# Kernel optimization log

Measured on AMD Instinct MI355X. Metric: run time of the kernel, lower is better.

Reference implementation:

```python
import jax, jax.numpy as jnp
import numpy as np

BN_EPS = 1e-5


def setup_inputs() -> dict:
    key = jax.random.key(0)
    ks = jax.random.split(key, 10)
    B, C, Ci, H, W = 4, 256, 128, 64, 64
    s = 0.05
    return {
        "x": jax.random.normal(ks[0], (B, C, H, W), jnp.float32),
        "g_w": jax.random.normal(ks[1], (Ci, C), jnp.float32) * s,
        "g_b": jax.random.normal(ks[2], (Ci,), jnp.float32) * s,
        "theta_w": jax.random.normal(ks[3], (Ci, C), jnp.float32) * s,
        "theta_b": jax.random.normal(ks[4], (Ci,), jnp.float32) * s,
        "phi_w": jax.random.normal(ks[5], (Ci, C), jnp.float32) * s,
        "phi_b": jax.random.normal(ks[6], (Ci,), jnp.float32) * s,
        "W_w": jax.random.normal(ks[7], (C, Ci), jnp.float32) * s,
        "W_b": jax.random.normal(ks[8], (C,), jnp.float32) * s,
        "bn_gamma": jnp.ones((C,), jnp.float32),
        "bn_beta": jnp.zeros((C,), jnp.float32),
        "scale": jax.random.normal(ks[9], (1,), jnp.float32),
    }


def reference(x, g_w, g_b, theta_w, theta_b, phi_w, phi_b, W_w, W_b, bn_gamma, bn_beta, scale):
    B, C, H, W = x.shape
    xf = x.reshape(B, C, H * W)  # [B, C, N]
    # 1x1 conv projections == channel matmuls
    g = jnp.einsum('oc,bcn->bno', g_w, xf) + g_b            # [B, N, Ci]
    th = jnp.einsum('oc,bcn->bno', theta_w, xf) + theta_b   # [B, N, Ci]
    ph = jnp.einsum('oc,bcn->bon', phi_w, xf) + phi_b[:, None]  # [B, Ci, N]
    # unscaled attention: f = theta @ phi, softmax over keys
    f = jnp.einsum('bnd,bdm->bnm', th, ph)                  # [B, N, N]
    attn = jax.nn.softmax(f, axis=-1)
    y = jnp.einsum('bnm,bmo->bno', attn, g)                 # [B, N, Ci]
    y4 = y.transpose(0, 2, 1).reshape(B, -1, H, W)          # [B, Ci, H, W]
    # W: 1x1 conv + BatchNorm2d (training mode: batch statistics)
    wy = jnp.einsum('od,bdhw->bohw', W_w, y4) + W_b[None, :, None, None]
    mean = wy.mean(axis=(0, 2, 3))
    var = wy.var(axis=(0, 2, 3))
    bn = (wy - mean[None, :, None, None]) * jax.lax.rsqrt(var[None, :, None, None] + BN_EPS)
    bn = bn * bn_gamma[None, :, None, None] + bn_beta[None, :, None, None]
    return scale * bn + x
```

## Files before the change

kernel.cpp:

```cpp
#include <hip/hip_runtime.h>
#include <hip/hip_bf16.h>

#define BB 4
#define CC 256
#define CI 128
#define NN 4096

typedef _Float16 f16;
typedef __attribute__((ext_vector_type(8))) _Float16 f16x8;
typedef __attribute__((ext_vector_type(4))) _Float16 f16x4;
typedef __attribute__((ext_vector_type(4))) float f32x4;

#define MFMA(a,b,c) __builtin_amdgcn_mfma_f32_16x16x32_f16(a,b,c,0,0,0)
#define LDS3(p) ((__attribute__((address_space(3))) void*)(p))
#define GL1(p)  ((const __attribute__((address_space(1))) void*)(p))

__global__ __launch_bounds__(256) void k01_xpose(const float* x, f16* xt,
                                                 const float* tw, const float* pw,
                                                 const float* gw, const float* Ww, f16* wdst){
    int nt = blockIdx.x, ct = blockIdx.y, b = blockIdx.z;
    __shared__ float tile[64][65];
    int t = threadIdx.x;
    const float* src = x + ((size_t)(b*CC + ct*64))*NN + nt*64;
    #pragma unroll
    for (int k=0;k<16;k++){ int idx=t+k*256; int cl=idx>>6, nl=idx&63;
        tile[cl][nl]=src[(size_t)cl*NN + nl]; }
    __syncthreads();
    f16* dst = xt + ((size_t)(b*NN + nt*64))*CC + ct*64;
    #pragma unroll
    for (int k=0;k<16;k++){ int idx=t+k*256; int nl=idx>>6, cl=idx&63;
        dst[(size_t)nl*CC + cl] = (f16)tile[cl][nl]; }
    if (t < 128){
        int blkId = blockIdx.x + 64*(blockIdx.y + 4*blockIdx.z);
        int i = blkId*128 + t;
        int j = i & 32767; int sel = i >> 15;
        const float* s = (sel==0)? tw : (sel==1)? pw : (sel==2)? gw : Ww;
        wdst[i] = (f16)s[j];
    }
}

__global__ __launch_bounds__(256) void k2_all(const f16* xt, const f16* thw, const f16* phw,
                                              const f16* gwh, const float* thb, const float* phb,
                                              const float* gb, f16* th, f16* ph, f16* gt2){
    int b = blockIdx.y; int xx = blockIdx.x;
    int wv = threadIdx.x>>6, lane = threadIdx.x&63, q=lane>>4, cc=lane&15;
    if (xx < 64){
        int mat = xx>>5; int ntile = xx&31;
        int n0 = ntile*128 + wv*32;
        f16x8 aq[2][8];
        #pragma unroll
        for (int ns=0;ns<2;ns++){
            const f16* ap = xt + ((size_t)(b*NN + n0 + ns*16 + cc))*CC + q*8;
            #pragma unroll
            for (int kk=0;kk<8;kk++) aq[ns][kk] = *(const f16x8*)(ap + kk*32);
        }
        const f16* w   = mat? phw : thw;
        const float* bias = mat? phb : thb;
        f16* o = mat? ph : th;
        #pragma unroll 1
        for (int os=0;os<8;os++){
            f32x4 acc0={0,0,0,0}, acc1={0,0,0,0};
            const f16* wp = w + ((size_t)(os*16 + cc))*CC + q*8;
            #pragma unroll
            for (int kk=0;kk<8;kk++){
                f16x8 bf = *(const f16x8*)(wp + kk*32);
                acc0 = MFMA(aq[0][kk], bf, acc0);
                acc1 = MFMA(aq[1][kk], bf, acc1);
            }
            float bv = bias[os*16+cc];
            #pragma unroll
            for (int r=0;r<4;r++){
                o[((size_t)(b*NN + n0      + 4*q + r))*CI + os*16 + cc] = (f16)(acc0[r] + bv);
                o[((size_t)(b*NN + n0 + 16 + 4*q + r))*CI + os*16 + cc] = (f16)(acc1[r] + bv);
            }
        }
    } else {
        int mt = xx - 64;
        f16x8 ag[2][8];
        #pragma unroll
        for (int os=0;os<2;os++){
            const f16* ap = gwh + ((size_t)(wv*32 + os*16 + cc))*CC + q*8;
            #pragma unroll
            for (int kk=0;kk<8;kk++) ag[os][kk] = *(const f16x8*)(ap + kk*32);
        }
        f32x4 acc[2][4];
        #pragma unroll
        for (int os=0;os<2;os++){
            #pragma unroll
            for (int ms=0;ms<4;ms++) acc[os][ms]=(f32x4){0,0,0,0};
        }
        #pragma unroll 1
        for (int kk=0;kk<8;kk++){
            #pragma unroll
            for (int ms=0;ms<4;ms++){
                f16x8 bf = *(const f16x8*)(xt + ((size_t)(b*NN + mt*64 + ms*16 + cc))*CC + kk*32 + q*8);
                acc[0][ms]=MFMA(ag[0][kk],bf,acc[0][ms]);
                acc[1][ms]=MFMA(ag[1][kk],bf,acc[1][ms]);
            }
        }
        #pragma unroll
        for (int os=0;os<2;os++){
            #pragma unroll
            for (int r=0;r<4;r++){
                int orow = wv*32 + os*16 + 4*q + r;
                float bv = gb[orow];
                #pragma unroll
                for (int ms=0;ms<4;ms++){
                    int pos = (ms>>1)*32 + 8*(cc>>2) + 4*(ms&1) + (cc&3);
                    gt2[((size_t)(b*64 + mt))*8192 + orow*64 + pos] = (f16)(acc[os][ms][r] + bv);
                }
            }
        }
    }
}

__global__ __launch_bounds__(256, 4) void k3_attn(const f16* th, const f16* ph, const f16* gt2,
                                                  f16* ypart, float* ml){
    int qt = blockIdx.x;
    int sp = blockIdx.y;
    int b  = blockIdx.z;
    int wv=threadIdx.x>>6, lane=threadIdx.x&63, q=lane>>4, cc=lane&15;
    int qrow0 = qt*64 + wv*16;
    int kv0 = sp*1024;
    int sw  = (cc&7)<<4;
    int sw2 = ((cc>>1)&3)<<4;

    __shared__ __align__(16) char ldsb[32768];
    char* phL = ldsb;
    char* gtL = ldsb + 16384;

    f16x8 aq[4];
    const f16* thp = th + ((size_t)(b*NN + qrow0 + cc))*CI + q*8;
    #pragma unroll
    for (int kk=0;kk<4;kk++) aq[kk] = *(const f16x8*)(thp + kk*32);

    const char* phg = (const char*)(ph + (size_t)b*NN*CI);
    const char* gtg = (const char*)gt2 + (size_t)b*64*16384;

    f32x4 yacc[8];
    #pragma unroll
    for (int os=0;os<8;os++) yacc[os]=(f32x4){0,0,0,0};
    float m_run = -1e30f;
    float l_run = 0.f;

    auto STAGE = [&](int tt, int bb){
        int key0 = kv0 + tt*32;
        int mt  = key0 >> 6;
        int kob = (key0 & 32)*2;
        char* pbase = phL + bb*8192 + wv*2048;
        char* gbase = gtL + bb*8192 + wv*2048;
        #pragma unroll
        for (int ch=0; ch<2; ch++){
            int prow = wv*8 + ch*4 + (lane>>4);
            const char* ps = phg + (size_t)(key0 + prow)*256 + (((lane&15)*16) ^ ((prow&7)<<4));
            __builtin_amdgcn_global_load_lds(GL1(ps), LDS3(pbase + ch*1024), 16, 0, 0);
            int gf = wv*2048 + ch*1024 + lane*16;
            int grow = gf>>6, gcol = gf&63;
            const char* gs = gtg + (size_t)mt*16384 + grow*128 + kob + (gcol ^ (((grow>>1)&3)<<4));
            __builtin_amdgcn_global_load_lds(GL1(gs), LDS3(gbase + ch*1024), 16, 0, 0);
        }
    };

    STAGE(0, 0);
    __syncthreads();

    int cur = 0;
    #pragma unroll 1
    for (int it=0; it<32; ++it){
        if (it < 31) STAGE(it+1, cur^1);
        const char* pt  = phL + cur*8192;
        const char* gtt = gtL + cur*8192;
        f32x4 fa[2];
        #pragma unroll
        for (int j=0;j<2;j++){
            f16x8 pf[4];
            #pragma unroll
            for (int kk=0;kk<4;kk++)
                pf[kk] = *(const f16x8*)(pt + (j*16+cc)*256 + ((kk*64 + q*16) ^ sw));
            fa[j]=(f32x4){0,0,0,0};
            #pragma unroll
            for (int kk=0;kk<4;kk++)
                fa[j]=MFMA(pf[kk], aq[kk], fa[j]);
        }
        float t0 = fmaxf(fmaxf(fa[0][0],fa[0][1]), fmaxf(fa[0][2],fa[0][3]));
        float t1 = fmaxf(fmaxf(fa[1][0],fa[1][1]), fmaxf(fa[1][2],fa[1][3]));
        float m0 = fmaxf(t0,t1);
        m0 = fmaxf(m0, __shfl_xor(m0,16));
        m0 = fmaxf(m0, __shfl_xor(m0,32));
        if (__any(m0 - m_run > 3.f)){
            float nm = fmaxf(m_run, m0);
            float co = __expf(m_run - nm);
            m_run = nm;
            l_run *= co;
            #pragma unroll
            for (int os=0;os<8;os++) yacc[os] *= co;
        }
        #pragma unroll
        for (int j=0;j<2;j++){
            #pragma unroll
            for (int r=0;r<4;r++) fa[j][r] = __expf(fa[j][r]-m_run);
        }
        l_run += ((fa[0][0]+fa[0][1])+(fa[0][2]+fa[0][3]))
               + ((fa[1][0]+fa[1][1])+(fa[1][2]+fa[1][3]));
        f16x8 pb;
        #pragma unroll
        for (int r=0;r<4;r++){ pb[r]=(f16)fa[0][r]; pb[4+r]=(f16)fa[1][r]; }
        #pragma unroll
        for (int os=0;os<8;os++){
            int row = os*16 + cc;
            f16x8 ga = *(const f16x8*)(gtt + row*64 + ((q*16) ^ sw2));
            yacc[os] = MFMA(ga, pb, yacc[os]);
        }
        __syncthreads();
        cur ^= 1;
    }
    float l = l_run;
    l += __shfl_xor(l,16);
    l += __shfl_xor(l,32);
    float linv = 1.f/l;
    f16* yl = (f16*)(ldsb + wv*4096);
    #pragma unroll
    for (int os=0;os<8;os++){
        #pragma unroll
        for (int r=0;r<4;r++){
            int o = os*16 + 4*q + r;
            *(f16*)((char*)yl + cc*256 + ((o*2) ^ ((cc&7)<<4))) = (f16)(yacc[os][r]*linv);
        }
    }
    #pragma unroll
    for (int p=0;p<4;p++){
        int idx = p*512 + lane*8;
        int row = idx>>7, o0 = idx&127;
        f16x8 v = *(const f16x8*)((char*)yl + row*256 + ((o0*2) ^ ((row&7)<<4)));
        *(f16x8*)(ypart + ((size_t)((sp*4+b)*NN + qrow0 + row))*CI + o0) = v;
    }
    if (lane < 16){
        size_t row = (size_t)(sp*4+b)*NN + qrow0 + lane;
        ml[row*2]   = m_run;
        ml[row*2+1] = l;
    }
}

__global__ __launch_bounds__(256) void k3c(const f16* ypart, const float* ml,
                                           f16* y, float* part, float* mupart){
    int blk = blockIdx.x; int t = threadIdx.x;
    int rloc = t>>2;
    int row  = blk*64 + rloc;
    int b = row>>12, n = row & 4095;
    int o0 = (t&3)*32;
    __shared__ __align__(16) f16 ldsT[128*64];
    float m_s[4], l_s[4];
    #pragma unroll
    for (int s=0;s<4;s++){ size_t r2 = ((size_t)(s*4+b)*NN + n)*2; m_s[s]=ml[r2]; l_s[s]=ml[r2+1]; }
    float M = fmaxf(fmaxf(m_s[0],m_s[1]),fmaxf(m_s[2],m_s[3]));
    float w[4]; float L=0.f;
    #pragma unroll
    for (int s=0;s<4;s++){ w[s]=l_s[s]*__expf(m_s[s]-M); L+=w[s]; }
    float inv = 1.f/L;
    #pragma unroll
    for (int s=0;s<4;s++) w[s]*=inv;
    float acc[32];
    #pragma unroll
    for (int j=0;j<32;j++) acc[j]=0.f;
    #pragma unroll
    for (int s=0;s<4;s++){
        const f16* src = ypart + ((size_t)(s*4+b)*NN + n)*CI + o0;
        #pragma unroll
        for (int v=0;v<4;v++){
            f16x8 vv = *(const f16x8*)(src + v*8);
            #pragma unroll
            for (int e=0;e<8;e++) acc[v*8+e] += w[s]*(float)vv[e];
        }
    }
    f16* yo = y + (size_t)row*CI + o0;
    #pragma unroll
    for (int v=0;v<4;v++){
        f16x8 ov;
        #pragma unroll
        for (int e=0;e<8;e++) ov[e] = (f16)acc[v*8+e];
        *(f16x8*)(yo + v*8) = ov;
        #pragma unroll
        for (int e=0;e<8;e++){
            int o = o0 + v*8 + e;
            ldsT[o*64 + (rloc ^ ((o&7)<<3))] = ov[e];
        }
    }
    __syncthreads();
    int wv=t>>6, lane=t&63, q=lane>>4, cc=lane&15;
    f32x4 gacc[2][8];
    #pragma unroll
    for (int a=0;a<2;a++)
        #pragma unroll
        for (int c2=0;c2<8;c2++) gacc[a][c2]=(f32x4){0,0,0,0};
    f16x8 af[2][2];
    #pragma unroll
    for (int o1t=0;o1t<2;o1t++){
        int o1 = (wv*2+o1t)*16+cc;
        #pragma unroll
        for (int kk=0;kk<2;kk++)
            af[o1t][kk] = *(const f16x8*)(ldsT + o1*64 + ((kk*32+q*8) ^ ((o1&7)<<3)));
    }
    #pragma unroll 1
    for (int o2t=0;o2t<8;o2t++){
        int o2 = o2t*16+cc;
        #pragma unroll
        for (int kk=0;kk<2;kk++){
            f16x8 bf = *(const f16x8*)(ldsT + o2*64 + ((kk*32+q*8) ^ ((o2&7)<<3)));
            gacc[0][o2t] = MFMA(af[0][kk], bf, gacc[0][o2t]);
            gacc[1][o2t] = MFMA(af[1][kk], bf, gacc[1][o2t]);
        }
    }
    float* pb = part + (size_t)blk*16384;
    #pragma unroll
    for (int o1t=0;o1t<2;o1t++){
        #pragma unroll
        for (int o2t=0;o2t<8;o2t++){
            #pragma unroll
            for (int r=0;r<4;r++)
                pb[((wv*2+o1t)*16+4*q+r)*128 + o2t*16+cc] = gacc[o1t][o2t][r];
        }
    }
    if (t<128){
        float sm=0.f;
        #pragma unroll
        for (int v=0;v<8;v++){
            f16x8 vv = *(const f16x8*)(ldsT + t*64 + ((v*8) ^ ((t&7)<<3)));
            #pragma unroll
            for (int e=0;e<8;e++) sm += (float)vv[e];
        }
        mupart[blk*128 + t] = sm;
    }
}

__global__ __launch_bounds__(256) void k4b_red(const float* part, const float* mupart, float* S){
    int pc = blockIdx.y;
    int t = threadIdx.x;
    if (blockIdx.x < 64){
        int i = blockIdx.x*256 + t;
        float s=0.f;
        #pragma unroll 1
        for (int p=pc*32; p<pc*32+32; p++) s += part[(size_t)p*16384 + i];
        atomicAdd(&S[i], s);
    } else if (t < 128){
        float s=0.f;
        #pragma unroll 1
        for (int p=pc*32; p<pc*32+32; p++) s += mupart[p*128 + t];
        atomicAdd(&S[16384+t], s);
    }
}

__global__ __launch_bounds__(128) void k4c_coef(const float* S, const float* Ww, const float* Wb,
                                                const float* gamma, const float* beta,
                                                const float* scale, float* AB){
    int ch = blockIdx.x; int t = threadIdx.x;
    const float* w = Ww + ch*CI;
    float tmp=0.f;
    const float* Srow = S + t*CI;
    #pragma unroll 1
    for (int o2=0;o2<CI;o2++) tmp += Srow[o2]*w[o2];
    float v  = w[t]*tmp;
    float mc = w[t]*S[16384 + t];
    #pragma unroll
    for (int s=1;s<64;s<<=1){ v += __shfl_xor(v,s); mc += __shfl_xor(mc,s); }
    __shared__ float red[4];
    if ((t&63)==0){ red[(t>>6)*2]=v; red[(t>>6)*2+1]=mc; }
    __syncthreads();
    if (t==0){
        float wSw = red[0]+red[2];
        float wmu = red[1]+red[3];
        const float M = 16384.f;
        float meanwy = wmu/M + Wb[ch];
        float var = wSw/M - (wmu/M)*(wmu/M);
        float inv = rsqrtf(var + 1e-5f);
        float sc = scale[0];
        float A  = sc*gamma[ch]*inv;
        float B3 = sc*(beta[ch] - meanwy*inv*gamma[ch]);
        AB[ch]     = A;
        AB[256+ch] = B3 + A*Wb[ch];
    }
}

__global__ __launch_bounds__(256) void k5_out(const f16* Wwh, const f16* y, const float* x,
                                              const float* AB, float* out){
    int ntile = blockIdx.x;
    int cht   = blockIdx.y;
    int b     = blockIdx.z;
    int wv=threadIdx.x>>6, lane=threadIdx.x&63, q=lane>>4, cc=lane&15;
    int ch0 = cht*64 + wv*16;
    f16x8 aw[4];
    const f16* wp = Wwh + ((size_t)(ch0+cc))*CI + q*8;
    #pragma unroll
    for (int kk=0;kk<4;kk++) aw[kk]=*(const f16x8*)(wp+kk*32);
    float Ar[4], Br[4];
    #pragma unroll
    for (int r=0;r<4;r++){ Ar[r]=AB[ch0+4*q+r]; Br[r]=AB[256+ch0+4*q+r]; }
    #pragma unroll 1
    for (int ns=0;ns<8;ns++){
        int n0 = ntile*128 + ns*16;
        f32x4 acc={0,0,0,0};
        const f16* yp = y + ((size_t)(b*NN + n0 + cc))*CI + q*8;
        #pragma unroll
        for (int kk=0;kk<4;kk++) acc = MFMA(aw[kk], *(const f16x8*)(yp+kk*32), acc);
        #pragma unroll
        for (int r=0;r<4;r++){
            size_t addr = ((size_t)(b*CC + ch0 + 4*q + r))*NN + n0 + cc;
            out[addr] = x[addr] + Ar[r]*acc[r] + Br[r];
        }
    }
}

extern "C" void kernel_launch(void* const* d_in, const int* in_sizes, int n_in,
                              void* d_out, int out_size, void* d_ws, size_t ws_size,
                              hipStream_t stream){
    const float* x    = (const float*)d_in[0];
    const float* g_w  = (const float*)d_in[1];
    const float* g_b  = (const float*)d_in[2];
    const float* th_w = (const float*)d_in[3];
    const float* th_b = (const float*)d_in[4];
    const float* ph_w = (const float*)d_in[5];
    const float* ph_b = (const float*)d_in[6];
    const float* W_w  = (const float*)d_in[7];
    const float* W_b  = (const float*)d_in[8];
    const float* bg   = (const float*)d_in[9];
    const float* bb   = (const float*)d_in[10];
    const float* sc   = (const float*)d_in[11];

    char* ws = (char*)d_ws;
    f16* xt  = (f16*)(ws);
    f16* th  = (f16*)(ws + 8388608);
    f16* ph  = (f16*)(ws + 8388608 + 1*4194304);
    f16* gt2 = (f16*)(ws + 8388608 + 2*4194304);
    f16* y   = (f16*)(ws + 8388608 + 3*4194304);
    f16* wh  = (f16*)(ws + 8388608 + 4*4194304);
    float* ml    = (float*)(ws + 25427968);
    f16*   ypart = (f16*)(ws + 25952256);
    float* mupart= (float*)(ws + 42729472);
    float* part  = (float*)ws;
    float* S    = (float*)(ws + 42860544);
    float* AB   = (float*)(ws + 42926592);
    f16* th_wh = wh;
    f16* ph_wh = wh + 32768;
    f16* g_wh  = wh + 65536;
    f16* Ww_h  = wh + 98304;

    hipMemsetAsync(S, 0, 16512*sizeof(float), stream);
    hipLaunchKernelGGL(k01_xpose, dim3(64,4,4), dim3(256), 0, stream, x, xt, th_w, ph_w, g_w, W_w, wh);
    hipLaunchKernelGGL(k2_all,   dim3(128,4),   dim3(256), 0, stream, xt, th_wh, ph_wh, g_wh,
                       th_b, ph_b, g_b, th, ph, gt2);
    hipLaunchKernelGGL(k3_attn,  dim3(64,4,4),  dim3(256), 0, stream, th, ph, gt2, ypart, ml);
    hipLaunchKernelGGL(k3c,      dim3(256),     dim3(256), 0, stream, ypart, ml, y, part, mupart);
    hipLaunchKernelGGL(k4b_red,  dim3(65,8),    dim3(256), 0, stream, part, mupart, S);
    hipLaunchKernelGGL(k4c_coef, dim3(256),     dim3(128), 0, stream, S, W_w, W_b, bg, bb, sc, AB);
    hipLaunchKernelGGL(k5_out,   dim3(32,4,4),  dim3(256), 0, stream, Ww_h, y, x, AB, (float*)d_out);
}
```

Before: 148.6 us.

## Double per-wave query rows and key tile in attention kernel for reuse

Each wave in the flash-attention kernel now processes 32 query rows, held as two 16-row blocks, instead of 16. Each loop iteration stages 64 keys instead of 32, with new LDS swizzles, so every phi and g fragment read from LDS feeds twice as many MFMAs and there are half as many barriers. The cost is twice the LDS (64KB), a bigger register footprint (occupancy hint lowered to 2), and half as many blocks in the grid. That can reduce latency hiding and load balance across CUs.

```diff
diff --git a/kernel.cpp b/kernel.cpp
--- a/kernel.cpp
+++ b/kernel.cpp
@@ -114,49 +114,54 @@
     }
 }
 
-__global__ __launch_bounds__(256, 4) void k3_attn(const f16* th, const f16* ph, const f16* gt2,
+__global__ __launch_bounds__(256, 2) void k3_attn(const f16* th, const f16* ph, const f16* gt2,
                                                   f16* ypart, float* ml){
     int qt = blockIdx.x;
     int sp = blockIdx.y;
     int b  = blockIdx.z;
     int wv=threadIdx.x>>6, lane=threadIdx.x&63, q=lane>>4, cc=lane&15;
-    int qrow0 = qt*64 + wv*16;
+    int qrow0 = qt*128 + wv*32;
     int kv0 = sp*1024;
-    int sw  = (cc&7)<<4;
-    int sw2 = ((cc>>1)&3)<<4;
-
-    __shared__ __align__(16) char ldsb[32768];
+    int sw  = cc<<4;
+    int hb  = (cc>>2)&1;
+    int c6  = (q*16) ^ (((cc>>3)&1)<<4);
+
+    __shared__ __align__(16) char ldsb[65536];
     char* phL = ldsb;
-    char* gtL = ldsb + 16384;
-
-    f16x8 aq[4];
-    const f16* thp = th + ((size_t)(b*NN + qrow0 + cc))*CI + q*8;
-    #pragma unroll
-    for (int kk=0;kk<4;kk++) aq[kk] = *(const f16x8*)(thp + kk*32);
+    char* gtL = ldsb + 32768;
+
+    f16x8 aq[2][4];
+    #pragma unroll
+    for (int rb=0;rb<2;rb++){
+        const f16* thp = th + ((size_t)(b*NN + qrow0 + rb*16 + cc))*CI + q*8;
+        #pragma unroll
+        for (int kk=0;kk<4;kk++) aq[rb][kk] = *(const f16x8*)(thp + kk*32);
+    }
 
     const char* phg = (const char*)(ph + (size_t)b*NN*CI);
     const char* gtg = (const char*)gt2 + (size_t)b*64*16384;
 
-    f32x4 yacc[8];
-    #pragma unroll
-    for (int os=0;os<8;os++) yacc[os]=(f32x4){0,0,0,0};
-    float m_run = -1e30f;
-    float l_run = 0.f;
+    f32x4 yacc[2][8];
+    #pragma unroll
+    for (int rb=0;rb<2;rb++)
+        #pragma unroll
+        for (int os=0;os<8;os++) yacc[rb][os]=(f32x4){0,0,0,0};
+    float m_run0=-1e30f, m_run1=-1e30f, l_run0=0.f, l_run1=0.f;
 
     auto STAGE = [&](int tt, int bb){
-        int key0 = kv0 + tt*32;
+        int key0 = kv0 + tt*64;
         int mt  = key0 >> 6;
-        int kob = (key0 & 32)*2;
-        char* pbase = phL + bb*8192 + wv*2048;
-        char* gbase = gtL + bb*8192 + wv*2048;
-        #pragma unroll
-        for (int ch=0; ch<2; ch++){
-            int prow = wv*8 + ch*4 + (lane>>4);
-            const char* ps = phg + (size_t)(key0 + prow)*256 + (((lane&15)*16) ^ ((prow&7)<<4));
+        char* pbase = phL + bb*16384 + wv*4096;
+        char* gbase = gtL + bb*16384 + wv*4096;
+        #pragma unroll
+        for (int ch=0; ch<4; ch++){
+            int prow = wv*16 + ch*4 + (lane>>4);
+            const char* ps = phg + (size_t)(key0 + prow)*256 + (((lane&15)*16) ^ ((prow&15)<<4));
             __builtin_amdgcn_global_load_lds(GL1(ps), LDS3(pbase + ch*1024), 16, 0, 0);
-            int gf = wv*2048 + ch*1024 + lane*16;
-            int grow = gf>>6, gcol = gf&63;
-            const char* gs = gtg + (size_t)mt*16384 + grow*128 + kob + (gcol ^ (((grow>>1)&3)<<4));
+            int gf = wv*4096 + ch*1024 + lane*16;
+            int grow = gf>>7, gcol = gf&127;
+            int scol = (((gcol>>6) ^ ((grow>>2)&1))<<6) | ((gcol&63) ^ (((grow>>3)&1)<<4));
+            const char* gs = gtg + (size_t)mt*16384 + grow*128 + scol;
             __builtin_amdgcn_global_load_lds(GL1(gs), LDS3(gbase + ch*1024), 16, 0, 0);
         }
     };
@@ -166,78 +171,110 @@
 
     int cur = 0;
     #pragma unroll 1
-    for (int it=0; it<32; ++it){
-        if (it < 31) STAGE(it+1, cur^1);
-        const char* pt  = phL + cur*8192;
-        const char* gtt = gtL + cur*8192;
-        f32x4 fa[2];
-        #pragma unroll
-        for (int j=0;j<2;j++){
+    for (int it=0; it<16; ++it){
+        if (it < 15) STAGE(it+1, cur^1);
+        const char* pt  = phL + cur*16384;
+        const char* gtt = gtL + cur*16384;
+        f32x4 fa[2][4];
+        #pragma unroll
+        for (int j=0;j<4;j++){
             f16x8 pf[4];
             #pragma unroll
             for (int kk=0;kk<4;kk++)
                 pf[kk] = *(const f16x8*)(pt + (j*16+cc)*256 + ((kk*64 + q*16) ^ sw));
-            fa[j]=(f32x4){0,0,0,0};
-            #pragma unroll
-            for (int kk=0;kk<4;kk++)
-                fa[j]=MFMA(pf[kk], aq[kk], fa[j]);
-        }
-        float t0 = fmaxf(fmaxf(fa[0][0],fa[0][1]), fmaxf(fa[0][2],fa[0][3]));
-        float t1 = fmaxf(fmaxf(fa[1][0],fa[1][1]), fmaxf(fa[1][2],fa[1][3]));
-        float m0 = fmaxf(t0,t1);
-        m0 = fmaxf(m0, __shfl_xor(m0,16));
-        m0 = fmaxf(m0, __shfl_xor(m0,32));
-        if (__any(m0 - m_run > 3.f)){
-            float nm = fmaxf(m_run, m0);
-            float co = __expf(m_run - nm);
-            m_run = nm;
-            l_run *= co;
-            #pragma unroll
-            for (int os=0;os<8;os++) yacc[os] *= co;
-        }
-        #pragma unroll
-        for (int j=0;j<2;j++){
-            #pragma unroll
-            for (int r=0;r<4;r++) fa[j][r] = __expf(fa[j][r]-m_run);
-        }
-        l_run += ((fa[0][0]+fa[0][1])+(fa[0][2]+fa[0][3]))
-               + ((fa[1][0]+fa[1][1])+(fa[1][2]+fa[1][3]));
-        f16x8 pb;
-        #pragma unroll
-        for (int r=0;r<4;r++){ pb[r]=(f16)fa[0][r]; pb[4+r]=(f16)fa[1][r]; }
+            fa[0][j]=(f32x4){0,0,0,0}; fa[1][j]=(f32x4){0,0,0,0};
+            #pragma unroll
+            for (int kk=0;kk<4;kk++){
+                fa[0][j]=MFMA(pf[kk], aq[0][kk], fa[0][j]);
+                fa[1][j]=MFMA(pf[kk], aq[1][kk], fa[1][j]);
+            }
+        }
+        float mA0 = fmaxf(fmaxf(fa[0][0][0],fa[0][0][1]),fmaxf(fa[0][0][2],fa[0][0][3]));
+        float mA1 = fmaxf(fmaxf(fa[0][1][0],fa[0][1][1]),fmaxf(fa[0][1][2],fa[0][1][3]));
+        float mA2 = fmaxf(fmaxf(fa[0][2][0],fa[0][2][1]),fmaxf(fa[0][2][2],fa[0][2][3]));
+        float mA3 = fmaxf(fmaxf(fa[0][3][0],fa[0][3][1]),fmaxf(fa[0][3][2],fa[0][3][3]));
+        float mx0 = fmaxf(fmaxf(mA0,mA1),fmaxf(mA2,mA3));
+        mx0 = fmaxf(mx0, __shfl_xor(mx0,16));
+        mx0 = fmaxf(mx0, __shfl_xor(mx0,32));
+        float mB0 = fmaxf(fmaxf(fa[1][0][0],fa[1][0][1]),fmaxf(fa[1][0][2],fa[1][0][3]));
+        float mB1 = fmaxf(fmaxf(fa[1][1][0],fa[1][1][1]),fmaxf(fa[1][1][2],fa[1][1][3]));
+        float mB2 = fmaxf(fmaxf(fa[1][2][0],fa[1][2][1]),fmaxf(fa[1][2][2],fa[1][2][3]));
+        float mB3 = fmaxf(fmaxf(fa[1][3][0],fa[1][3][1]),fmaxf(fa[1][3][2],fa[1][3][3]));
+        float mx1 = fmaxf(fmaxf(mB0,mB1),fmaxf(mB2,mB3));
+        mx1 = fmaxf(mx1, __shfl_xor(mx1,16));
+        mx1 = fmaxf(mx1, __shfl_xor(mx1,32));
+        float need = fmaxf(mx0 - m_run0, mx1 - m_run1);
+        if (__any(need > 3.f)){
+            float nm0 = fmaxf(m_run0, mx0), nm1 = fmaxf(m_run1, mx1);
+            float co0 = __expf(m_run0 - nm0), co1 = __expf(m_run1 - nm1);
+            m_run0 = nm0; m_run1 = nm1;
+            l_run0 *= co0; l_run1 *= co1;
+            #pragma unroll
+            for (int os=0;os<8;os++){ yacc[0][os] *= co0; yacc[1][os] *= co1; }
+        }
+        #pragma unroll
+        for (int j=0;j<4;j++){
+            #pragma unroll
+            for (int r=0;r<4;r++){
+                fa[0][j][r] = __expf(fa[0][j][r]-m_run0);
+                fa[1][j][r] = __expf(fa[1][j][r]-m_run1);
+            }
+        }
+        l_run0 += ((fa[0][0][0]+fa[0][0][1]+fa[0][0][2]+fa[0][0][3])
+                 + (fa[0][1][0]+fa[0][1][1]+fa[0][1][2]+fa[0][1][3]))
+                + ((fa[0][2][0]+fa[0][2][1]+fa[0][2][2]+fa[0][2][3])
+                 + (fa[0][3][0]+fa[0][3][1]+fa[0][3][2]+fa[0][3][3]));
+        l_run1 += ((fa[1][0][0]+fa[1][0][1]+fa[1][0][2]+fa[1][0][3])
+                 + (fa[1][1][0]+fa[1][1][1]+fa[1][1][2]+fa[1][1][3]))
+                + ((fa[1][2][0]+fa[1][2][1]+fa[1][2][2]+fa[1][2][3])
+                 + (fa[1][3][0]+fa[1][3][1]+fa[1][3][2]+fa[1][3][3]));
+        f16x8 pb0h0, pb0h1, pb1h0, pb1h1;
+        #pragma unroll
+        for (int r=0;r<4;r++){
+            pb0h0[r]=(f16)fa[0][0][r]; pb0h0[4+r]=(f16)fa[0][1][r];
+            pb0h1[r]=(f16)fa[0][2][r]; pb0h1[4+r]=(f16)fa[0][3][r];
+            pb1h0[r]=(f16)fa[1][0][r]; pb1h0[4+r]=(f16)fa[1][1][r];
+            pb1h1[r]=(f16)fa[1][2][r]; pb1h1[4+r]=(f16)fa[1][3][r];
+        }
         #pragma unroll
         for (int os=0;os<8;os++){
             int row = os*16 + cc;
-            f16x8 ga = *(const f16x8*)(gtt + row*64 + ((q*16) ^ sw2));
-            yacc[os] = MFMA(ga, pb, yacc[os]);
+            f16x8 ga0 = *(const f16x8*)(gtt + row*128 + ((hb    )<<6) + c6);
+            f16x8 ga1 = *(const f16x8*)(gtt + row*128 + ((1 ^ hb)<<6) + c6);
+            yacc[0][os] = MFMA(ga0, pb0h0, yacc[0][os]);
+            yacc[1][os] = MFMA(ga0, pb1h0, yacc[1][os]);
+            yacc[0][os] = MFMA(ga1, pb0h1, yacc[0][os]);
+            yacc[1][os] = MFMA(ga1, pb1h1, yacc[1][os]);
         }
         __syncthreads();
         cur ^= 1;
     }
-    float l = l_run;
-    l += __shfl_xor(l,16);
-    l += __shfl_xor(l,32);
-    float linv = 1.f/l;
-    f16* yl = (f16*)(ldsb + wv*4096);
+    float l0 = l_run0; l0 += __shfl_xor(l0,16); l0 += __shfl_xor(l0,32);
+    float l1 = l_run1; l1 += __shfl_xor(l1,16); l1 += __shfl_xor(l1,32);
+    float linv0 = 1.f/l0, linv1 = 1.f/l1;
+    f16* yl = (f16*)(ldsb + wv*8192);
     #pragma unroll
     for (int os=0;os<8;os++){
         #pragma unroll
         for (int r=0;r<4;r++){
             int o = os*16 + 4*q + r;
-            *(f16*)((char*)yl + cc*256 + ((o*2) ^ ((cc&7)<<4))) = (f16)(yacc[os][r]*linv);
-        }
-    }
-    #pragma unroll
-    for (int p=0;p<4;p++){
+            *(f16*)((char*)yl + cc*256      + ((o*2) ^ ((cc&7)<<4))) = (f16)(yacc[0][os][r]*linv0);
+            *(f16*)((char*)yl + (16+cc)*256 + ((o*2) ^ ((cc&7)<<4))) = (f16)(yacc[1][os][r]*linv1);
+        }
+    }
+    #pragma unroll
+    for (int p=0;p<8;p++){
         int idx = p*512 + lane*8;
         int row = idx>>7, o0 = idx&127;
         f16x8 v = *(const f16x8*)((char*)yl + row*256 + ((o0*2) ^ ((row&7)<<4)));
         *(f16x8*)(ypart + ((size_t)((sp*4+b)*NN + qrow0 + row))*CI + o0) = v;
     }
     if (lane < 16){
-        size_t row = (size_t)(sp*4+b)*NN + qrow0 + lane;
-        ml[row*2]   = m_run;
-        ml[row*2+1] = l;
+        size_t row0 = (size_t)(sp*4+b)*NN + qrow0 + lane;
+        ml[row0*2]        = m_run0;
+        ml[row0*2+1]      = l0;
+        ml[(row0+16)*2]   = m_run1;
+        ml[(row0+16)*2+1] = l1;
     }
 }
 
@@ -447,7 +484,7 @@
     hipLaunchKernelGGL(k01_xpose, dim3(64,4,4), dim3(256), 0, stream, x, xt, th_w, ph_w, g_w, W_w, wh);
     hipLaunchKernelGGL(k2_all,   dim3(128,4),   dim3(256), 0, stream, xt, th_wh, ph_wh, g_wh,
                        th_b, ph_b, g_b, th, ph, gt2);
-    hipLaunchKernelGGL(k3_attn,  dim3(64,4,4),  dim3(256), 0, stream, th, ph, gt2, ypart, ml);
+    hipLaunchKernelGGL(k3_attn,  dim3(32,4,4),  dim3(256), 0, stream, th, ph, gt2, ypart, ml);
     hipLaunchKernelGGL(k3c,      dim3(256),     dim3(256), 0, stream, ypart, ml, y, part, mupart);
     hipLaunchKernelGGL(k4b_red,  dim3(65,8),    dim3(256), 0, stream, part, mupart, S);
     hipLaunchKernelGGL(k4c_coef, dim3(256),     dim3(128), 0, stream, S, W_w, W_b, bg, bb, sc, AB);
```

Measured after the change: 139.1 us. 6.4% less time.
